# Optimization experiments

Hardware: AMD Instinct MI355X
Metric: run time of the kernel (lower is better)

The kernel has to match this reference:

```python
import jax, jax.numpy as jnp
import numpy as np

B, S, D, H, E, K, DH = 4, 2048, 1024, 8, 8, 2, 128
ROPE_BASE = 10000.0


def setup_inputs() -> dict:
    key = jax.random.key(0)
    ks = jax.random.split(key, 7)
    s = 1.0 / np.sqrt(D)
    x = jax.random.normal(ks[0], (B, S, D), dtype=jnp.float32)
    Wq = jax.random.normal(ks[1], (H * DH, D), dtype=jnp.float32) * s
    Wk = jax.random.normal(ks[2], (H * DH, D), dtype=jnp.float32) * s
    Wv = jax.random.normal(ks[3], (H * E, D, DH), dtype=jnp.float32) * s
    Wo = jax.random.normal(ks[4], (H * E, DH, D), dtype=jnp.float32) * (1.0 / np.sqrt(H * DH))
    sel_v = jax.random.normal(ks[5], (H * E, D), dtype=jnp.float32) * s
    sel_o = jax.random.normal(ks[6], (H * E, D), dtype=jnp.float32) * s
    positions = jnp.broadcast_to(jnp.arange(S, dtype=jnp.int32), (B, S))
    return {"x": x, "Wq": Wq, "Wk": Wk, "Wv": Wv, "Wo": Wo,
            "sel_v": sel_v, "sel_o": sel_o, "positions": positions}


def _rope(t, pos, inv_freq):
    # t: [b,h,s,d], pos: [b,s]
    freqs = pos.astype(t.dtype)[:, :, None] * inv_freq          # [b,s,d/2]
    emb = jnp.concatenate([freqs, freqs], axis=-1)[:, None]      # [b,1,s,d]
    sin, cos = jnp.sin(emb), jnp.cos(emb)
    x1, x2 = jnp.split(t, 2, axis=-1)
    rot = jnp.concatenate([-x2, x1], axis=-1)
    return t * cos + rot * sin


def reference(x, Wq, Wk, Wv, Wo, sel_v, sel_o, positions):
    # dense shared Q/K projections -> [b,h,s,dh]
    q = (x @ Wq.T).reshape(B, S, H, DH).transpose(0, 2, 1, 3)
    k = (x @ Wk.T).reshape(B, S, H, DH).transpose(0, 2, 1, 3)

    # V expert routing (sigmoid, non-competitive top-k per head)
    gv = jax.nn.sigmoid((x @ sel_v.T).reshape(B, S, H, E))       # [b,s,h,e]
    vw, vi = jax.lax.top_k(gv, K)                                # [b,s,h,k]
    vall = jnp.einsum('bsm,hemd->bshed', x, Wv.reshape(H, E, D, DH))
    vsel = jnp.take_along_axis(vall, vi[..., None], axis=3)      # [b,s,h,k,dh]
    v = (vw[..., None] * vsel).sum(axis=3).transpose(0, 2, 1, 3)  # [b,h,s,dh]

    # RoPE (rotate_fraction=1 -> full head dim)
    inv_freq = 1.0 / (ROPE_BASE ** (jnp.arange(0, DH, 2, dtype=jnp.float32) / DH))
    q = _rope(q, positions, inv_freq)
    k = _rope(k, positions, inv_freq)

    # masked SDPA (causal bool mask, scale 1/sqrt(dh))
    scores = jnp.einsum('bhqd,bhkd->bhqk', q, k) * (1.0 / np.sqrt(DH))
    causal = jnp.tril(jnp.ones((S, S), dtype=bool))
    scores = jnp.where(causal, scores, jnp.finfo(scores.dtype).min)
    attn = jax.nn.softmax(scores, axis=-1)
    ctx = jnp.einsum('bhqk,bhkd->bqhd', attn, v)                  # [b,s,h,dh]

    # O expert routing, combine via scattered gate weights
    go = jax.nn.sigmoid((x @ sel_o.T).reshape(B, S, H, E))
    ow, oi = jax.lax.top_k(go, K)
    g_full = (ow[..., None] * jax.nn.one_hot(oi, E, dtype=x.dtype)).sum(axis=3)  # [b,s,h,e]
    out = jnp.einsum('bshd,bshe,hedm->bsm', ctx, g_full, Wo.reshape(H, E, DH, D))
    return out
```

## Files before the change

### kernel.cpp

```cpp
#include <hip/hip_runtime.h>
#include <math.h>

typedef unsigned short u16;
typedef unsigned int u32;
typedef __attribute__((ext_vector_type(8))) short short8;
typedef __attribute__((ext_vector_type(4))) float f32x4;

constexpr int cB = 4, cS = 2048, cD = 1024, cH = 8, cE = 8, cK = 2, cDH = 128;
constexpr int cBS = cB * cS;
constexpr int cHE = cH * cE;

__device__ inline u16 f2bf(float f) {
    u32 u = __float_as_uint(f);
    u += 0x7fffu + ((u >> 16) & 1u);
    return (u16)(u >> 16);
}
__device__ inline float bf2f(u16 h) { return __uint_as_float(((u32)h) << 16); }

__device__ inline void gload_lds16(const u16* g, u16* l) {
    __builtin_amdgcn_global_load_lds(
        (const __attribute__((address_space(1))) void*)g,
        (__attribute__((address_space(3))) void*)l, 16, 0, 0);
}

#define SWZ_RD(row, ks, quad) ((((quad) + ((ks) >> 3)) ^ ((row) & 7)) << 3)

__global__ __launch_bounds__(256) void k_cast_split(
    const float* __restrict__ src, u16* __restrict__ hi, u16* __restrict__ lo)
{
    const size_t i = (size_t)blockIdx.x * 256 + threadIdx.x;
    float4 v = ((const float4*)src)[i];
    u16 hx = f2bf(v.x), hy = f2bf(v.y), hz = f2bf(v.z), hw = f2bf(v.w);
    u16 lx = f2bf(v.x - bf2f(hx)), ly = f2bf(v.y - bf2f(hy));
    u16 lz = f2bf(v.z - bf2f(hz)), lw = f2bf(v.w - bf2f(hw));
    uint2 oh; oh.x = (u32)hx | ((u32)hy << 16); oh.y = (u32)hz | ((u32)hw << 16);
    uint2 ol; ol.x = (u32)lx | ((u32)ly << 16); ol.y = (u32)lz | ((u32)lw << 16);
    ((uint2*)hi)[i] = oh;
    ((uint2*)lo)[i] = ol;
}

__global__ __launch_bounds__(256, 2) void k_gemm_logits3(
    const u16* __restrict__ xh, const u16* __restrict__ xlo,
    const u16* __restrict__ selh, const u16* __restrict__ sell,
    float* __restrict__ lgp)
{
    __shared__ u16 As[128 * 64];
    __shared__ u16 Bs[128 * 64];
    const int r0 = blockIdx.x * 128;
    const int term = blockIdx.y;
    const u16* A = (term == 1) ? xlo : xh;
    const u16* B = (term == 2) ? sell : selh;
    float* outp = lgp + (size_t)term * cBS * 128;
    const int t = threadIdx.x;
    const int w = t >> 6, lane = t & 63;
    const int wm = w >> 1, wn = w & 1;
    const int quad = lane >> 4, lm = lane & 15;
    const int lr = lane >> 3;
    const int lcs = (((lane & 7) ^ lr) * 8);

    f32x4 acc[4][4];
#pragma unroll
    for (int i = 0; i < 4; i++)
#pragma unroll
        for (int j = 0; j < 4; j++)
#pragma unroll
            for (int r = 0; r < 4; r++) acc[i][j][r] = 0.0f;

    for (int kc = 0; kc < cD; kc += 64) {
#pragma unroll
        for (int p = 0; p < 4; p++) {
            const int rA = p * 32 + w * 8;
            gload_lds16(A + (size_t)(r0 + rA + lr) * cD + kc + lcs, As + rA * 64);
            gload_lds16(B + (size_t)(rA + lr) * cD + kc + lcs, Bs + rA * 64);
        }
        __syncthreads();
#pragma unroll
        for (int ks = 0; ks < 64; ks += 32) {
            short8 av[4], bv[4];
#pragma unroll
            for (int i = 0; i < 4; i++) {
                const int row = wm * 64 + i * 16 + lm;
                av[i] = *(const short8*)(As + row * 64 + SWZ_RD(row, ks, quad));
            }
#pragma unroll
            for (int j = 0; j < 4; j++) {
                const int row = wn * 64 + j * 16 + lm;
                bv[j] = *(const short8*)(Bs + row * 64 + SWZ_RD(row, ks, quad));
            }
#pragma unroll
            for (int i = 0; i < 4; i++)
#pragma unroll
                for (int j = 0; j < 4; j++)
                    acc[i][j] = __builtin_amdgcn_mfma_f32_16x16x32_bf16(av[i], bv[j], acc[i][j], 0, 0, 0);
        }
        __syncthreads();
    }
#pragma unroll
    for (int i = 0; i < 4; i++)
#pragma unroll
        for (int r = 0; r < 4; r++) {
            const int row = r0 + wm * 64 + i * 16 + quad * 4 + r;
#pragma unroll
            for (int j = 0; j < 4; j++)
                outp[(size_t)row * 128 + wn * 64 + j * 16 + lm] = acc[i][j][r];
        }
}

__global__ __launch_bounds__(256) void k_top2_flag(
    const float* __restrict__ lgp, float* __restrict__ gv_d, float* __restrict__ go_d,
    int* __restrict__ flags, int* __restrict__ counter)
{
    const int idx = blockIdx.x * 256 + threadIdx.x;
    const int row = idx >> 4, r16 = idx & 15;
    const int which = r16 >> 3, h = r16 & 7;
    const float* l0 = lgp + (size_t)row * 128 + which * 64 + h * 8;
    const float* l1 = l0 + (size_t)cBS * 128;
    const float* l2 = l1 + (size_t)cBS * 128;
    float v[8];
#pragma unroll
    for (int e = 0; e < cE; e++) v[e] = l0[e] + l1[e] + l2[e];
    int i0 = 0; float b0 = v[0];
#pragma unroll
    for (int e = 1; e < cE; e++) { if (v[e] > b0) { b0 = v[e]; i0 = e; } }
    int i1 = -1; float b1 = -3.0e38f;
#pragma unroll
    for (int e = 0; e < cE; e++) { if (e != i0 && v[e] > b1) { b1 = v[e]; i1 = e; } }
    float b2 = -3.0e38f;
#pragma unroll
    for (int e = 0; e < cE; e++) { if (e != i0 && e != i1 && v[e] > b2) b2 = v[e]; }
    const float w0 = 1.0f / (1.0f + __expf(-b0));
    const float w1 = 1.0f / (1.0f + __expf(-b1));
    float* dst = (which ? go_d : gv_d) + (size_t)row * 64 + h * 8;
#pragma unroll
    for (int e = 0; e < cE; e++)
        dst[e] = (e == i0) ? w0 : ((e == i1) ? w1 : 0.0f);
    if (b1 - b2 < 1.0e-3f) {
        const int s = atomicAdd(counter, 1);
        flags[s] = (row << 4) | r16;
    }
}

__global__ __launch_bounds__(64) void k_repair(
    const float* __restrict__ x, const float* __restrict__ sel_v,
    const float* __restrict__ sel_o,
    const int* __restrict__ counter, const int* __restrict__ flags,
    float* __restrict__ gv_d, float* __restrict__ go_d)
{
    const int n = *counter;
    const int lane = threadIdx.x;
    for (int it = blockIdx.x; it < n; it += gridDim.x) {
        const int item = flags[it];
        const int row = item >> 4, which = (item >> 3) & 1, h = item & 7;
        const float* xr = x + (size_t)row * cD;
        const float* sb = (which ? sel_o : sel_v) + (size_t)(h * 8) * cD;
        float lg[8];
#pragma unroll
        for (int e = 0; e < cE; e++) {
            float a = 0.0f;
#pragma unroll
            for (int dg = 0; dg < 4; dg++) {
                const int d = dg * 256 + lane * 4;
                const float4 xv = *(const float4*)(xr + d);
                const float4 sv = *(const float4*)(sb + (size_t)e * cD + d);
                a += xv.x * sv.x + xv.y * sv.y + xv.z * sv.z + xv.w * sv.w;
            }
#pragma unroll
            for (int off = 1; off < 64; off <<= 1) a += __shfl_xor(a, off);
            lg[e] = a;
        }
        int i0 = 0; float b0 = lg[0];
#pragma unroll
        for (int e = 1; e < cE; e++) { if (lg[e] > b0) { b0 = lg[e]; i0 = e; } }
        int i1 = -1; float b1 = -3.0e38f;
#pragma unroll
        for (int e = 0; e < cE; e++) { if (e != i0 && lg[e] > b1) { b1 = lg[e]; i1 = e; } }
        if (lane == 0) {
            const float w0 = 1.0f / (1.0f + expf(-b0));
            const float w1 = 1.0f / (1.0f + expf(-b1));
            float* dst = (which ? go_d : gv_d) + (size_t)row * 64 + h * 8;
#pragma unroll
            for (int e = 0; e < cE; e++)
                dst[e] = (e == i0) ? w0 : ((e == i1) ? w1 : 0.0f);
        }
    }
}

__global__ __launch_bounds__(256) void k_cast_f2b(
    const float* __restrict__ src, u16* __restrict__ dst)
{
    const size_t i = (size_t)blockIdx.x * 256 + threadIdx.x;
    float4 v = ((const float4*)src)[i];
    u32 lo = (u32)f2bf(v.x) | ((u32)f2bf(v.y) << 16);
    u32 hi = (u32)f2bf(v.z) | ((u32)f2bf(v.w) << 16);
    uint2 o; o.x = lo; o.y = hi;
    ((uint2*)dst)[i] = o;
}

__global__ __launch_bounds__(256) void k_cast_wv(
    const float* __restrict__ Wv, u16* __restrict__ WvT)
{
    __shared__ float ld[64][132];
    const int d0 = blockIdx.x * 64, he = blockIdx.y;
    const int t = threadIdx.x;
    for (int p = 0; p < 8; p++) {
        const int slot = p * 256 + t, r = slot >> 5, c4 = slot & 31;
        float4 v = *(const float4*)(Wv + ((size_t)he * cD + d0 + r) * cDH + c4 * 4);
        ld[r][c4 * 4 + 0] = v.x; ld[r][c4 * 4 + 1] = v.y;
        ld[r][c4 * 4 + 2] = v.z; ld[r][c4 * 4 + 3] = v.w;
    }
    __syncthreads();
    for (int p = 0; p < 16; p++) {
        const int slot = p * 256 + t, dh = slot >> 5, c2 = slot & 31;
        u32 val = (u32)f2bf(ld[c2 * 2 + 0][dh]) | ((u32)f2bf(ld[c2 * 2 + 1][dh]) << 16);
        *(u32*)(WvT + (size_t)(he * cDH + dh) * cD + d0 + c2 * 2) = val;
    }
}

__global__ __launch_bounds__(256) void k_cast_wo(
    const float* __restrict__ Wo, u16* __restrict__ WoT)
{
    __shared__ float ld[128][68];
    const int m0 = blockIdx.x * 64, he = blockIdx.y;
    const int t = threadIdx.x;
    for (int p = 0; p < 8; p++) {
        const int slot = p * 256 + t, r = slot >> 4, c4 = slot & 15;
        float4 v = *(const float4*)(Wo + ((size_t)he * cDH + r) * cD + m0 + c4 * 4);
        ld[r][c4 * 4 + 0] = v.x; ld[r][c4 * 4 + 1] = v.y;
        ld[r][c4 * 4 + 2] = v.z; ld[r][c4 * 4 + 3] = v.w;
    }
    __syncthreads();
    for (int p = 0; p < 16; p++) {
        const int slot = p * 256 + t, mr = slot >> 6, c2 = slot & 63;
        u32 val = (u32)f2bf(ld[c2 * 2 + 0][mr]) | ((u32)f2bf(ld[c2 * 2 + 1][mr]) << 16);
        *(u32*)(WoT + (size_t)(m0 + mr) * 8192 + he * cDH + c2 * 2) = val;
    }
}

__global__ __launch_bounds__(256, 2) void k_gemm_v(
    const u16* __restrict__ xh, const u16* __restrict__ WvT,
    const float* __restrict__ gv_d, u16* __restrict__ v_b)
{
    __shared__ u16 As[128 * 72];
    __shared__ u16 Bs[128 * 72];
    __shared__ float Gs[128][9];
    const int rt = blockIdx.x, h = blockIdx.y;
    const int r0 = rt * 128;
    const int t = threadIdx.x;
    const int w = t >> 6, lane = t & 63;
    const int wm = w >> 1, wn = w & 1;
    const int quad = lane >> 4, lm = lane & 15;

    {
        const int row = t >> 1, half = t & 1;
        float4 g4 = *(const float4*)(gv_d + (size_t)(r0 + row) * 64 + h * 8 + half * 4);
        Gs[row][half * 4 + 0] = g4.x; Gs[row][half * 4 + 1] = g4.y;
        Gs[row][half * 4 + 2] = g4.z; Gs[row][half * 4 + 3] = g4.w;
    }

    f32x4 acc[4][4];
#pragma unroll
    for (int i = 0; i < 4; i++)
#pragma unroll
        for (int j = 0; j < 4; j++)
#pragma unroll
            for (int r = 0; r < 4; r++) acc[i][j][r] = 0.0f;

    for (int e = 0; e < cE; e++) {
        f32x4 acce[4][4];
#pragma unroll
        for (int i = 0; i < 4; i++)
#pragma unroll
            for (int j = 0; j < 4; j++)
#pragma unroll
                for (int r = 0; r < 4; r++) acce[i][j][r] = 0.0f;

        for (int kc = 0; kc < cD; kc += 64) {
#pragma unroll
            for (int p = 0; p < 4; p++) {
                const int slot = p * 256 + t, row = slot >> 3, seg = slot & 7;
                *(uint4*)(As + row * 72 + seg * 8) =
                    *(const uint4*)(xh + (size_t)(r0 + row) * cD + kc + seg * 8);
                *(uint4*)(Bs + row * 72 + seg * 8) =
                    *(const uint4*)(WvT + (size_t)((h * 8 + e) * cDH + row) * cD + kc + seg * 8);
            }
            __syncthreads();
#pragma unroll
            for (int ks = 0; ks < 64; ks += 32) {
                short8 av[4], bv[4];
#pragma unroll
                for (int i = 0; i < 4; i++)
                    av[i] = *(const short8*)(As + (wm * 64 + i * 16 + lm) * 72 + ks + quad * 8);
#pragma unroll
                for (int j = 0; j < 4; j++)
                    bv[j] = *(const short8*)(Bs + (wn * 64 + j * 16 + lm) * 72 + ks + quad * 8);
#pragma unroll
                for (int i = 0; i < 4; i++)
#pragma unroll
                    for (int j = 0; j < 4; j++)
                        acce[i][j] = __builtin_amdgcn_mfma_f32_16x16x32_bf16(av[i], bv[j], acce[i][j], 0, 0, 0);
            }
            __syncthreads();
        }
#pragma unroll
        for (int i = 0; i < 4; i++)
#pragma unroll
            for (int r = 0; r < 4; r++) {
                const float g = Gs[wm * 64 + i * 16 + quad * 4 + r][e];
#pragma unroll
                for (int j = 0; j < 4; j++) acc[i][j][r] += g * acce[i][j][r];
            }
    }
#pragma unroll
    for (int i = 0; i < 4; i++)
#pragma unroll
        for (int r = 0; r < 4; r++) {
            const int row = r0 + wm * 64 + i * 16 + quad * 4 + r;
            const int b = row >> 11, s = row & (cS - 1);
            u16* dst = v_b + ((size_t)(b * cH + h) * cS + s) * cDH;
#pragma unroll
            for (int j = 0; j < 4; j++)
                dst[wn * 64 + j * 16 + lm] = f2bf(acc[i][j][r]);
        }
}

__global__ __launch_bounds__(256, 2) void k_gemm_o(
    const u16* __restrict__ ctxh, const u16* __restrict__ WoT,
    const float* __restrict__ go_d, float* __restrict__ out)
{
    __shared__ u16 As[2][128 * 64];
    __shared__ u16 Bs[2][128 * 64];
    __shared__ float Gs[128][9];
    const int rt = blockIdx.x, nt = blockIdx.y;
    const int r0 = rt * 128;
    const int t = threadIdx.x;
    const int w = t >> 6, lane = t & 63;
    const int wm = w >> 1, wn = w & 1;
    const int quad = lane >> 4, lm = lane & 15;
    const int lr = lane >> 3;
    const int lcs = (((lane & 7) ^ lr) * 8);

    f32x4 acc[4][4];
#pragma unroll
    for (int i = 0; i < 4; i++)
#pragma unroll
        for (int j = 0; j < 4; j++)
#pragma unroll
            for (int r = 0; r < 4; r++) acc[i][j][r] = 0.0f;

    for (int h = 0; h < cH; h++) {
        for (int e = 0; e < cE; e++) {
            const int he = h * 8 + e;
            if (e == 0) {
#pragma unroll
                for (int kc = 0; kc < 2; kc++)
#pragma unroll
                    for (int p = 0; p < 4; p++) {
                        const int rA = p * 32 + w * 8;
                        gload_lds16(ctxh + (size_t)(r0 + rA + lr) * cD + h * 128 + kc * 64 + lcs,
                                    As[kc] + rA * 64);
                    }
                const int row = t >> 1, half = t & 1;
                float4 g4 = *(const float4*)(go_d + (size_t)(r0 + row) * 64 + h * 8 + half * 4);
                Gs[row][half * 4 + 0] = g4.x; Gs[row][half * 4 + 1] = g4.y;
                Gs[row][half * 4 + 2] = g4.z; Gs[row][half * 4 + 3] = g4.w;
            }
#pragma unroll
            for (int kc = 0; kc < 2; kc++)
#pragma unroll
                for (int p = 0; p < 4; p++) {
                    const int rA = p * 32 + w * 8;
                    gload_lds16(WoT + (size_t)(nt * 128 + rA + lr) * 8192 + he * 128 + kc * 64 + lcs,
                                Bs[kc] + rA * 64);
                }
            __syncthreads();

            f32x4 acce[4][4];
#pragma unroll
            for (int i = 0; i < 4; i++)
#pragma unroll
                for (int j = 0; j < 4; j++)
#pragma unroll
                    for (int r = 0; r < 4; r++) acce[i][j][r] = 0.0f;
#pragma unroll
            for (int kc = 0; kc < 2; kc++)
#pragma unroll
                for (int ks = 0; ks < 64; ks += 32) {
                    short8 av[4], bv[4];
#pragma unroll
                    for (int i = 0; i < 4; i++) {
                        const int row = wm * 64 + i * 16 + lm;
                        av[i] = *(const short8*)(As[kc] + row * 64 + SWZ_RD(row, ks, quad));
                    }
#pragma unroll
                    for (int j = 0; j < 4; j++) {
                        const int row = wn * 64 + j * 16 + lm;
                        bv[j] = *(const short8*)(Bs[kc] + row * 64 + SWZ_RD(row, ks, quad));
                    }
#pragma unroll
                    for (int i = 0; i < 4; i++)
#pragma unroll
                        for (int j = 0; j < 4; j++)
                            acce[i][j] = __builtin_amdgcn_mfma_f32_16x16x32_bf16(av[i], bv[j], acce[i][j], 0, 0, 0);
                }
#pragma unroll
            for (int i = 0; i < 4; i++)
#pragma unroll
                for (int r = 0; r < 4; r++) {
                    const float g = Gs[wm * 64 + i * 16 + quad * 4 + r][e];
#pragma unroll
                    for (int j = 0; j < 4; j++) acc[i][j][r] += g * acce[i][j][r];
                }
            __syncthreads();
        }
    }
#pragma unroll
    for (int i = 0; i < 4; i++)
#pragma unroll
        for (int r = 0; r < 4; r++) {
            const int row = r0 + wm * 64 + i * 16 + quad * 4 + r;
            float* dst = out + (size_t)row * cD + nt * 128;
#pragma unroll
            for (int j = 0; j < 4; j++)
                dst[wn * 64 + j * 16 + lm] = acc[i][j][r];
        }
}

__global__ __launch_bounds__(256, 2) void k_qkproj_mfma(
    const u16* __restrict__ xh, const u16* __restrict__ Wqb,
    const u16* __restrict__ Wkb, float* __restrict__ q_t, float* __restrict__ k_t)
{
    __shared__ u16 As[128 * 64];
    __shared__ u16 Bs[128 * 64];
    const int rt = blockIdx.x, nt = blockIdx.y;
    const bool isK = nt >= cH;
    const int h = isK ? nt - cH : nt;
    const u16* Wb = isK ? Wkb : Wqb;
    float* outp = isK ? k_t : q_t;
    const int r0 = rt * 128;
    const int t = threadIdx.x;
    const int w = t >> 6, lane = t & 63;
    const int wm = w >> 1, wn = w & 1;
    const int quad = lane >> 4, lm = lane & 15;
    const int lr = lane >> 3;
    const int lcs = (((lane & 7) ^ lr) * 8);

    f32x4 acc[4][4];
#pragma unroll
    for (int i = 0; i < 4; i++)
#pragma unroll
        for (int j = 0; j < 4; j++)
#pragma unroll
            for (int r = 0; r < 4; r++) acc[i][j][r] = 0.0f;

    for (int kc = 0; kc < cD; kc += 64) {
#pragma unroll
        for (int p = 0; p < 4; p++) {
            const int rA = p * 32 + w * 8;
            gload_lds16(xh + (size_t)(r0 + rA + lr) * cD + kc + lcs, As + rA * 64);
            gload_lds16(Wb + (size_t)(h * cDH + rA + lr) * cD + kc + lcs, Bs + rA * 64);
        }
        __syncthreads();
#pragma unroll
        for (int ks = 0; ks < 64; ks += 32) {
            short8 av[4], bv[4];
#pragma unroll
            for (int i = 0; i < 4; i++) {
                const int row = wm * 64 + i * 16 + lm;
                av[i] = *(const short8*)(As + row * 64 + SWZ_RD(row, ks, quad));
            }
#pragma unroll
            for (int j = 0; j < 4; j++) {
                const int row = wn * 64 + j * 16 + lm;
                bv[j] = *(const short8*)(Bs + row * 64 + SWZ_RD(row, ks, quad));
            }
#pragma unroll
            for (int i = 0; i < 4; i++)
#pragma unroll
                for (int j = 0; j < 4; j++)
                    acc[i][j] = __builtin_amdgcn_mfma_f32_16x16x32_bf16(av[i], bv[j], acc[i][j], 0, 0, 0);
        }
        __syncthreads();
    }
#pragma unroll
    for (int i = 0; i < 4; i++)
#pragma unroll
        for (int r = 0; r < 4; r++) {
            const int row = r0 + wm * 64 + i * 16 + quad * 4 + r;
            const int b = row >> 11, s = row & (cS - 1);
            float* dst = outp + ((size_t)(b * cH + h) * cS + s) * cDH;
#pragma unroll
            for (int j = 0; j < 4; j++)
                dst[wn * 64 + j * 16 + lm] = acc[i][j][r];
        }
}

__global__ __launch_bounds__(256) void k_rope_cast(
    const float* __restrict__ q_t, const float* __restrict__ k_t,
    const int* __restrict__ positions,
    u16* __restrict__ q_b, u16* __restrict__ k_b)
{
    const int total = cB * cH * cS * (cDH / 2);
    const int idx = blockIdx.x * 256 + threadIdx.x;
    const int which = (idx >= total) ? 1 : 0;
    const int id = which ? idx - total : idx;
    const int i = id & 63;
    const int bhs = id >> 6;
    const int s = bhs & (cS - 1);
    const int b = (bhs >> 11) >> 3;
    const float* src = (which ? k_t : q_t) + (size_t)bhs * cDH;
    u16* dst = (which ? k_b : q_b) + (size_t)bhs * cDH;
    const int pos = positions[b * cS + s];
    const float freq = exp2f((float)i * -0.20762050593745932f);
    const float ang = (float)pos * freq;
    float sn, c;
    __sincosf(ang, &sn, &c);
    const float t1 = src[i], t2 = src[i + 64];
    dst[i] = f2bf(t1 * c - t2 * sn);
    dst[i + 64] = f2bf(t2 * c + t1 * sn);
}

__global__ __launch_bounds__(256, 2) void k_attn_mfma(
    const u16* __restrict__ qb, const u16* __restrict__ kb,
    const u16* __restrict__ vb, u16* __restrict__ ctxh)
{
    __shared__ u16 Ks[64][136];
    __shared__ u16 VsT[128][72];
    __shared__ u16 Ps[4][32][72];

    const int combined = blockIdx.z * 8 + blockIdx.y;
    const int qtv = (combined < 16) ? (15 - (int)blockIdx.x) : (int)blockIdx.x;
    const int h = blockIdx.y, b = blockIdx.z;
    const int q0 = qtv * 128;
    const int t = threadIdx.x;
    const int w = t >> 6, lane = t & 63;
    const int quad = lane >> 4, lm = lane & 15;
    const size_t bh = (size_t)(b * cH + h) * cS;
    const u16* kbase = kb + bh * cDH;
    const u16* vbase = vb + bh * cDH;

    short8 aq[2][4];
#pragma unroll
    for (int mi = 0; mi < 2; mi++) {
        const u16* qrow = qb + (bh + q0 + w * 32 + mi * 16 + lm) * cDH;
#pragma unroll
        for (int ks = 0; ks < 4; ks++)
            aq[mi][ks] = *(const short8*)(qrow + ks * 32 + quad * 8);
    }

    f32x4 o_acc[2][8];
#pragma unroll
    for (int mi = 0; mi < 2; mi++)
#pragma unroll
        for (int j = 0; j < 8; j++)
#pragma unroll
            for (int r = 0; r < 4; r++) o_acc[mi][j][r] = 0.0f;
    float m_r[2][4], l_r[2][4];
#pragma unroll
    for (int mi = 0; mi < 2; mi++)
#pragma unroll
        for (int r = 0; r < 4; r++) { m_r[mi][r] = -1.0e30f; l_r[mi][r] = 0.0f; }
    const float scale = 0.08838834764831845f;
    const int nkt = 2 * qtv + 2;

    for (int kt = 0; kt < nkt; kt++) {
        const int k0 = kt * 64;
#pragma unroll
        for (int p = 0; p < 4; p++) {
            const int slot = p * 256 + t, row = slot >> 4, seg = slot & 15;
            *(uint4*)&Ks[row][seg * 8] =
                *(const uint4*)(kbase + (size_t)(k0 + row) * cDH + seg * 8);
        }
        {
            const int rq = t & 15, seg = t >> 4;
            uint4 r0v = *(const uint4*)(vbase + (size_t)(k0 + rq * 4 + 0) * cDH + seg * 8);
            uint4 r1v = *(const uint4*)(vbase + (size_t)(k0 + rq * 4 + 1) * cDH + seg * 8);
            uint4 r2v = *(const uint4*)(vbase + (size_t)(k0 + rq * 4 + 2) * cDH + seg * 8);
            uint4 r3v = *(const uint4*)(vbase + (size_t)(k0 + rq * 4 + 3) * cDH + seg * 8);
            const u16* p0 = (const u16*)&r0v; const u16* p1 = (const u16*)&r1v;
            const u16* p2 = (const u16*)&r2v; const u16* p3 = (const u16*)&r3v;
#pragma unroll
            for (int jj = 0; jj < 8; jj++) {
                ushort4 val;
                val.x = p0[jj]; val.y = p1[jj]; val.z = p2[jj]; val.w = p3[jj];
                *(ushort4*)&VsT[seg * 8 + jj][rq * 4] = val;
            }
        }
        __syncthreads();

        f32x4 s[2][4];
#pragma unroll
        for (int mi = 0; mi < 2; mi++)
#pragma unroll
            for (int j = 0; j < 4; j++)
#pragma unroll
                for (int r = 0; r < 4; r++) s[mi][j][r] = 0.0f;
        __builtin_amdgcn_s_setprio(1);
#pragma unroll
        for (int ks = 0; ks < 4; ks++) {
#pragma unroll
            for (int j = 0; j < 4; j++) {
                short8 bv = *(const short8*)&Ks[j * 16 + lm][ks * 32 + quad * 8];
                s[0][j] = __builtin_amdgcn_mfma_f32_16x16x32_bf16(aq[0][ks], bv, s[0][j], 0, 0, 0);
                s[1][j] = __builtin_amdgcn_mfma_f32_16x16x32_bf16(aq[1][ks], bv, s[1][j], 0, 0, 0);
            }
        }
        __builtin_amdgcn_s_setprio(0);
        if (kt >= nkt - 2) {
#pragma unroll
            for (int mi = 0; mi < 2; mi++)
#pragma unroll
                for (int j = 0; j < 4; j++) {
                    const int colg = k0 + j * 16 + lm;
#pragma unroll
                    for (int r = 0; r < 4; r++) {
                        const int rowg = q0 + w * 32 + mi * 16 + quad * 4 + r;
                        s[mi][j][r] = (colg <= rowg) ? s[mi][j][r] * scale : -1.0e30f;
                    }
                }
        } else {
#pragma unroll
            for (int mi = 0; mi < 2; mi++)
#pragma unroll
                for (int j = 0; j < 4; j++)
#pragma unroll
                    for (int r = 0; r < 4; r++) s[mi][j][r] *= scale;
        }
#pragma unroll
        for (int mi = 0; mi < 2; mi++) {
            float mt[4];
#pragma unroll
            for (int r = 0; r < 4; r++)
                mt[r] = fmaxf(fmaxf(s[mi][0][r], s[mi][1][r]), fmaxf(s[mi][2][r], s[mi][3][r]));
#pragma unroll
            for (int off = 1; off < 16; off <<= 1)
#pragma unroll
                for (int r = 0; r < 4; r++) mt[r] = fmaxf(mt[r], __shfl_xor(mt[r], off));
            float alpha[4], rs[4];
#pragma unroll
            for (int r = 0; r < 4; r++) {
                const float mn = fmaxf(m_r[mi][r], mt[r]);
                alpha[r] = __expf(m_r[mi][r] - mn);
                m_r[mi][r] = mn;
                rs[r] = 0.0f;
            }
#pragma unroll
            for (int j = 0; j < 4; j++)
#pragma unroll
                for (int r = 0; r < 4; r++) {
                    const float p = __expf(s[mi][j][r] - m_r[mi][r]);
                    s[mi][j][r] = p;
                    rs[r] += p;
                }
#pragma unroll
            for (int off = 1; off < 16; off <<= 1)
#pragma unroll
                for (int r = 0; r < 4; r++) rs[r] += __shfl_xor(rs[r], off);
#pragma unroll
            for (int r = 0; r < 4; r++) l_r[mi][r] = l_r[mi][r] * alpha[r] + rs[r];
#pragma unroll
            for (int j = 0; j < 8; j++)
#pragma unroll
                for (int r = 0; r < 4; r++) o_acc[mi][j][r] *= alpha[r];
#pragma unroll
            for (int j = 0; j < 4; j++)
#pragma unroll
                for (int r = 0; r < 4; r++)
                    Ps[w][mi * 16 + quad * 4 + r][j * 16 + lm] = f2bf(s[mi][j][r]);
        }
        __builtin_amdgcn_s_setprio(1);
#pragma unroll
        for (int ks2 = 0; ks2 < 2; ks2++) {
            short8 ap0 = *(const short8*)&Ps[w][lm][ks2 * 32 + quad * 8];
            short8 ap1 = *(const short8*)&Ps[w][16 + lm][ks2 * 32 + quad * 8];
#pragma unroll
            for (int j2 = 0; j2 < 8; j2++) {
                short8 bv = *(const short8*)&VsT[j2 * 16 + lm][ks2 * 32 + quad * 8];
                o_acc[0][j2] = __builtin_amdgcn_mfma_f32_16x16x32_bf16(ap0, bv, o_acc[0][j2], 0, 0, 0);
                o_acc[1][j2] = __builtin_amdgcn_mfma_f32_16x16x32_bf16(ap1, bv, o_acc[1][j2], 0, 0, 0);
            }
        }
        __builtin_amdgcn_s_setprio(0);
        __syncthreads();
    }
#pragma unroll
    for (int mi = 0; mi < 2; mi++)
#pragma unroll
        for (int r = 0; r < 4; r++) {
            const float inv = 1.0f / l_r[mi][r];
            const int sg = q0 + w * 32 + mi * 16 + quad * 4 + r;
            u16* dst = ctxh + (((size_t)b * cS + sg) * cH + h) * cDH;
#pragma unroll
            for (int j2 = 0; j2 < 8; j2++)
                dst[j2 * 16 + lm] = f2bf(o_acc[mi][j2][r] * inv);
        }
}

extern "C" void kernel_launch(void* const* d_in, const int* in_sizes, int n_in,
                              void* d_out, int out_size, void* d_ws, size_t ws_size,
                              hipStream_t stream)
{
    const float* x = (const float*)d_in[0];
    const float* Wq = (const float*)d_in[1];
    const float* Wk = (const float*)d_in[2];
    const float* Wv = (const float*)d_in[3];
    const float* Wo = (const float*)d_in[4];
    const float* sel_v = (const float*)d_in[5];
    const float* sel_o = (const float*)d_in[6];
    const int* positions = (const int*)d_in[7];
    float* out = (float*)d_out;

    char* ws = (char*)d_ws;
    size_t off = 0;
    auto alloc = [&](size_t bytes) -> void* {
        void* p = ws + off;
        off += (bytes + 255) & ~(size_t)255;
        return p;
    };
    const size_t big = (size_t)cB * cH * cS * cDH * sizeof(float);
    const size_t half = big / 2;
    char* R1 = (char*)alloc(big);
    char* R2 = (char*)alloc(big);
    char* R3 = (char*)alloc(big);
    char* R4 = (char*)alloc(big);
    float* gv_d = (float*)alloc((size_t)cBS * 64 * sizeof(float));
    float* go_d = (float*)alloc((size_t)cBS * 64 * sizeof(float));
    u16* selh = (u16*)alloc((size_t)128 * cD * sizeof(u16));
    u16* sell = (u16*)alloc((size_t)128 * cD * sizeof(u16));
    int* flags = (int*)alloc((size_t)cBS * 16 * sizeof(int));
    int* counter = (int*)alloc(256);

    u16* WvT = (u16*)R1;
    float* lgp = (float*)(R1 + half);
    float* q_t = (float*)R1;
    u16* xlo = (u16*)R2;
    float* k_t = (float*)R2;
    u16* WoT = (u16*)R2;
    u16* v_b = (u16*)R3;
    u16* Wqb = (u16*)(R3 + half);
    u16* Wkb = (u16*)(R3 + half + ((size_t)cD * cD * 2));
    u16* ctxh = (u16*)(R3 + half);
    u16* xh = (u16*)R4;
    u16* q_b = (u16*)R4;
    u16* k_b = (u16*)(R4 + half);

    hipMemsetAsync(counter, 0, sizeof(int), stream);

    k_cast_split<<<8192, 256, 0, stream>>>(x, xh, xlo);
    k_cast_split<<<64, 256, 0, stream>>>(sel_v, selh, sell);
    k_cast_split<<<64, 256, 0, stream>>>(sel_o, selh + (size_t)cHE * cD,
                                         sell + (size_t)cHE * cD);
    k_gemm_logits3<<<dim3(64, 3), 256, 0, stream>>>(xh, xlo, selh, sell, lgp);
    k_top2_flag<<<512, 256, 0, stream>>>(lgp, gv_d, go_d, flags, counter);
    k_repair<<<256, 64, 0, stream>>>(x, sel_v, sel_o, counter, flags, gv_d, go_d);

    k_cast_wv<<<dim3(16, 64), 256, 0, stream>>>(Wv, WvT);
    k_gemm_v<<<dim3(64, 8), 256, 0, stream>>>(xh, WvT, gv_d, v_b);

    k_cast_f2b<<<1024, 256, 0, stream>>>(Wq, Wqb);
    k_cast_f2b<<<1024, 256, 0, stream>>>(Wk, Wkb);
    k_qkproj_mfma<<<dim3(64, 16), 256, 0, stream>>>(xh, Wqb, Wkb, q_t, k_t);
    k_rope_cast<<<(2 * cB * cH * cS * (cDH / 2)) / 256, 256, 0, stream>>>(
        q_t, k_t, positions, q_b, k_b);
    k_attn_mfma<<<dim3(16, 8, 4), 256, 0, stream>>>(q_b, k_b, v_b, ctxh);

    k_cast_wo<<<dim3(16, 64), 256, 0, stream>>>(Wo, WoT);
    k_gemm_o<<<dim3(64, 8), 256, 0, stream>>>(ctxh, WoT, go_d, out);
}
```

Before: 655.1 us.

## Double-buffer V expert GEMM with async global-to-LDS loads and swizzled layout

Rewrites the V projection GEMM main loop to flatten the expert and K-chunk loops into one tile loop, using two LDS buffers filled by direct global_load_lds instructions. The next tile is prefetched while MFMAs run on the current one, and the padded LDS layout is replaced by an XOR-swizzled one to avoid bank conflicts. This is meant to hide global-load latency and drop the register round-trip and one barrier per step. In exchange it doubles LDS use, which may limit occupancy, and it relies on a SWZ_RD macro defined elsewhere matching the write swizzle.

```diff
diff --git a/kernel.cpp b/kernel.cpp
--- a/kernel.cpp
+++ b/kernel.cpp
@@ -240,8 +240,8 @@
     const u16* __restrict__ xh, const u16* __restrict__ WvT,
     const float* __restrict__ gv_d, u16* __restrict__ v_b)
 {
-    __shared__ u16 As[128 * 72];
-    __shared__ u16 Bs[128 * 72];
+    __shared__ u16 As[2][128 * 64];
+    __shared__ u16 Bs[2][128 * 64];
     __shared__ float Gs[128][9];
     const int rt = blockIdx.x, h = blockIdx.y;
     const int r0 = rt * 128;
@@ -249,6 +249,8 @@
     const int w = t >> 6, lane = t & 63;
     const int wm = w >> 1, wn = w & 1;
     const int quad = lane >> 4, lm = lane & 15;
+    const int lr = lane >> 3;
+    const int lcs = (((lane & 7) ^ lr) * 8);
 
     {
         const int row = t >> 1, half = t & 1;
@@ -257,6 +259,17 @@
         Gs[row][half * 4 + 2] = g4.z; Gs[row][half * 4 + 3] = g4.w;
     }
 
+    auto stage = [&](int buf, int tile) {
+        const int e = tile >> 4, kc = (tile & 15) * 64;
+        const u16* Bbase = WvT + (size_t)((h * 8 + e) * cDH) * cD;
+#pragma unroll
+        for (int p = 0; p < 4; p++) {
+            const int rA = p * 32 + w * 8;
+            gload_lds16(xh + (size_t)(r0 + rA + lr) * cD + kc + lcs, As[buf] + rA * 64);
+            gload_lds16(Bbase + (size_t)(rA + lr) * cD + kc + lcs, Bs[buf] + rA * 64);
+        }
+    };
+
     f32x4 acc[4][4];
 #pragma unroll
     for (int i = 0; i < 4; i++)
@@ -264,51 +277,53 @@
         for (int j = 0; j < 4; j++)
 #pragma unroll
             for (int r = 0; r < 4; r++) acc[i][j][r] = 0.0f;
-
-    for (int e = 0; e < cE; e++) {
-        f32x4 acce[4][4];
-#pragma unroll
-        for (int i = 0; i < 4; i++)
-#pragma unroll
-            for (int j = 0; j < 4; j++)
-#pragma unroll
-                for (int r = 0; r < 4; r++) acce[i][j][r] = 0.0f;
-
-        for (int kc = 0; kc < cD; kc += 64) {
-#pragma unroll
-            for (int p = 0; p < 4; p++) {
-                const int slot = p * 256 + t, row = slot >> 3, seg = slot & 7;
-                *(uint4*)(As + row * 72 + seg * 8) =
-                    *(const uint4*)(xh + (size_t)(r0 + row) * cD + kc + seg * 8);
-                *(uint4*)(Bs + row * 72 + seg * 8) =
-                    *(const uint4*)(WvT + (size_t)((h * 8 + e) * cDH + row) * cD + kc + seg * 8);
-            }
-            __syncthreads();
-#pragma unroll
-            for (int ks = 0; ks < 64; ks += 32) {
-                short8 av[4], bv[4];
-#pragma unroll
-                for (int i = 0; i < 4; i++)
-                    av[i] = *(const short8*)(As + (wm * 64 + i * 16 + lm) * 72 + ks + quad * 8);
+    f32x4 acce[4][4];
+
+    stage(0, 0);
+    __syncthreads();
+
+    for (int tile = 0; tile < 128; tile++) {
+        const int cur = tile & 1;
+        if (tile < 127) stage(cur ^ 1, tile + 1);
+        if ((tile & 15) == 0) {
+#pragma unroll
+            for (int i = 0; i < 4; i++)
 #pragma unroll
                 for (int j = 0; j < 4; j++)
-                    bv[j] = *(const short8*)(Bs + (wn * 64 + j * 16 + lm) * 72 + ks + quad * 8);
-#pragma unroll
-                for (int i = 0; i < 4; i++)
-#pragma unroll
-                    for (int j = 0; j < 4; j++)
-                        acce[i][j] = __builtin_amdgcn_mfma_f32_16x16x32_bf16(av[i], bv[j], acce[i][j], 0, 0, 0);
-            }
-            __syncthreads();
-        }
-#pragma unroll
-        for (int i = 0; i < 4; i++)
-#pragma unroll
-            for (int r = 0; r < 4; r++) {
-                const float g = Gs[wm * 64 + i * 16 + quad * 4 + r][e];
-#pragma unroll
-                for (int j = 0; j < 4; j++) acc[i][j][r] += g * acce[i][j][r];
-            }
+#pragma unroll
+                    for (int r = 0; r < 4; r++) acce[i][j][r] = 0.0f;
+        }
+#pragma unroll
+        for (int ks = 0; ks < 64; ks += 32) {
+            short8 av[4], bv[4];
+#pragma unroll
+            for (int i = 0; i < 4; i++) {
+                const int row = wm * 64 + i * 16 + lm;
+                av[i] = *(const short8*)(As[cur] + row * 64 + SWZ_RD(row, ks, quad));
+            }
+#pragma unroll
+            for (int j = 0; j < 4; j++) {
+                const int row = wn * 64 + j * 16 + lm;
+                bv[j] = *(const short8*)(Bs[cur] + row * 64 + SWZ_RD(row, ks, quad));
+            }
+#pragma unroll
+            for (int i = 0; i < 4; i++)
+#pragma unroll
+                for (int j = 0; j < 4; j++)
+                    acce[i][j] = __builtin_amdgcn_mfma_f32_16x16x32_bf16(av[i], bv[j], acce[i][j], 0, 0, 0);
+        }
+        if ((tile & 15) == 15) {
+            const int e = tile >> 4;
+#pragma unroll
+            for (int i = 0; i < 4; i++)
+#pragma unroll
+                for (int r = 0; r < 4; r++) {
+                    const float g = Gs[wm * 64 + i * 16 + quad * 4 + r][e];
+#pragma unroll
+                    for (int j = 0; j < 4; j++) acc[i][j][r] += g * acce[i][j][r];
+                }
+        }
+        __syncthreads();
     }
 #pragma unroll
     for (int i = 0; i < 4; i++)
```

New measurement: 647.1 us. No clear change (-1.2%).
